# Optimization experiments

Measured on AMD Instinct MI355X. Metric: run time of the kernel, lower is better.

The kernel has to match this reference:

```python
import jax, jax.numpy as jnp
import numpy as np

B, T, D, H = 2, 2048, 1024, 16
DK = D // H

def setup_inputs() -> dict:
    key = jax.random.key(0)
    ks = jax.random.split(key, 12)
    s = 1.0 / np.sqrt(D)
    inp = {
        'Q': jax.random.normal(ks[0], (B, T, D), jnp.float32),
        'K': jax.random.normal(ks[1], (B, T, D), jnp.float32),
        'V': jax.random.normal(ks[2], (B, T, D), jnp.float32),
        'mask': jnp.tril(jnp.ones((T, T), jnp.int32))[None, None],  # causal [1,1,T,T]
        'Wq_w': jax.random.normal(ks[3], (D, D), jnp.float32) * s,
        'Wq_b': jax.random.normal(ks[4], (D,), jnp.float32) * s,
        'Wk_w': jax.random.normal(ks[5], (D, D), jnp.float32) * s,
        'Wk_b': jax.random.normal(ks[6], (D,), jnp.float32) * s,
        'Wv_w': jax.random.normal(ks[7], (D, D), jnp.float32) * s,
        'Wv_b': jax.random.normal(ks[8], (D,), jnp.float32) * s,
        'Wo_w': jax.random.normal(ks[9], (D, D), jnp.float32) * s,
        'Wo_b': jax.random.normal(ks[10], (D,), jnp.float32) * s,
    }
    return inp

def reference(Q, K, V, mask, Wq_w, Wq_b, Wk_w, Wk_b, Wv_w, Wv_b, Wo_w, Wo_b):
    b, tq, c = Q.shape
    tk = K.shape[1]
    q = (Q @ Wq_w + Wq_b).reshape(b, tq, H, DK).transpose(0, 2, 1, 3)  # [B,H,Tq,dk]
    k = (K @ Wk_w + Wk_b).reshape(b, tk, H, DK).transpose(0, 2, 1, 3)
    v = (V @ Wv_w + Wv_b).reshape(b, tk, H, DK).transpose(0, 2, 1, 3)
    scores = jnp.einsum('bhqd,bhkd->bhqk', q, k) / jnp.sqrt(jnp.float32(DK))
    scores = jnp.where(mask == 0, jnp.float32(-1e9), scores)
    attn = jax.nn.softmax(scores, axis=-1)
    out = jnp.einsum('bhqk,bhkd->bhqd', attn, v)
    out = out.transpose(0, 2, 1, 3).reshape(b, tq, c)
    return out @ Wo_w + Wo_b
```

## Files before the change

### kernel.cpp

```cpp
#include <hip/hip_runtime.h>
#include <hip/hip_bf16.h>

#define NB 2
#define NT 2048
#define ND 1024
#define NH 16
#define NDK 64

typedef __attribute__((ext_vector_type(8))) short bf16x8;
typedef __attribute__((ext_vector_type(4))) float f32x4;

#define VMCNT0 asm volatile("s_waitcnt vmcnt(0)" ::: "memory")
#define VMCNT3 asm volatile("s_waitcnt vmcnt(3)" ::: "memory")
#define VMCNT4 asm volatile("s_waitcnt vmcnt(4)" ::: "memory")

static __device__ __forceinline__ short f2bf(float f) {
  union { float f; unsigned u; } c; c.f = f;
  unsigned u = c.u;
  u += 0x7FFF + ((u >> 16) & 1);
  return (short)(u >> 16);
}

static __device__ __forceinline__ unsigned cvt_pk_bf16(float lo, float hi) {
  unsigned r;
  asm("v_cvt_pk_bf16_f32 %0, %1, %2" : "=v"(r) : "v"(lo), "v"(hi));
  return r;
}

static __device__ __forceinline__ void gload16(const void* g, void* l) {
  __builtin_amdgcn_global_load_lds((const __attribute__((address_space(1))) void*)g,
                                   (__attribute__((address_space(3))) void*)l, 16, 0, 0);
}

__global__ void prep_kernel(const float* __restrict__ Q, const float* __restrict__ Ki,
                            const float* __restrict__ V,
                            short* __restrict__ Qb, short* __restrict__ Kb, short* __restrict__ Vb,
                            const float* __restrict__ W0, const float* __restrict__ W1,
                            const float* __restrict__ W2, const float* __restrict__ W3,
                            short* __restrict__ T0, short* __restrict__ T1,
                            short* __restrict__ T2, short* __restrict__ T3) {
  __shared__ float t[32][33];
  int d = blockIdx.x, tid = threadIdx.x;
  if (d < 6144) {
    int z = d >> 11;
    int i = (d & 2047) * 256 + tid;
    const float* src = z == 0 ? Q : (z == 1 ? Ki : V);
    short* dst       = z == 0 ? Qb : (z == 1 ? Kb : Vb);
    const float4* s4 = (const float4*)src + (size_t)i * 2;
    float4 a = s4[0], b = s4[1];
    bf16x8 o;
    o[0] = f2bf(a.x); o[1] = f2bf(a.y); o[2] = f2bf(a.z); o[3] = f2bf(a.w);
    o[4] = f2bf(b.x); o[5] = f2bf(b.y); o[6] = f2bf(b.z); o[7] = f2bf(b.w);
    *((bf16x8*)dst + i) = o;
  } else {
    int dd = d - 6144;
    int z = dd >> 10;
    int rem = dd & 1023;
    const float* W = z == 0 ? W0 : (z == 1 ? W1 : (z == 2 ? W2 : W3));
    short* Wt      = z == 0 ? T0 : (z == 1 ? T1 : (z == 2 ? T2 : T3));
    int n0 = (rem & 31) * 32, k0 = (rem >> 5) * 32;
    int tx = tid & 31, ty = tid >> 5;
    for (int i = ty; i < 32; i += 8) t[i][tx] = W[(size_t)(k0 + i) * ND + n0 + tx];
    __syncthreads();
    for (int i = ty; i < 32; i += 8) Wt[(size_t)(n0 + i) * ND + k0 + tx] = f2bf(t[tx][i]);
  }
}

template <int MODE, int BN>
__global__ __launch_bounds__(256, 3) void gemm_bt(
    const short* __restrict__ A0, const short* __restrict__ A1, const short* __restrict__ A2,
    const short* __restrict__ W0, const short* __restrict__ W1, const short* __restrict__ W2,
    const float* __restrict__ b0, const float* __restrict__ b1, const float* __restrict__ b2,
    void* o0, void* o1, void* o2)
{
  constexpr int K = ND;
  constexpr int NK = K / 32;
  constexpr int NI = BN / 32;
  constexpr int NNB = ND / BN;
  constexpr int NZ = (MODE == 0) ? 3 : 1;
  constexpr int NWPX = NZ * 32 * NNB / 8;
  __shared__ short As[3][128 * 32];
  __shared__ short Bs[3][BN * 32];

  int d = blockIdx.x;
  int work = (d & 7) * NWPX + (d >> 3);
  int z = work / (32 * NNB);
  int rem = work % (32 * NNB);
  int m0 = (rem / NNB) * 128, n0 = (rem % NNB) * BN;

  const short* A    = z == 0 ? A0 : (z == 1 ? A1 : A2);
  const short* Wt   = z == 0 ? W0 : (z == 1 ? W1 : W2);
  const float* bias = z == 0 ? b0 : (z == 1 ? b1 : b2);
  void* out         = z == 0 ? o0 : (z == 1 ? o1 : o2);
  float scl = (MODE == 0 && z == 0) ? 0.18033688011112042f : 1.0f;

  int tid = threadIdx.x, wid = tid >> 6, lane = tid & 63;
  int wr = wid >> 1, wc = wid & 1;
  int r16 = lane & 15, l4 = lane >> 4;

  auto stage = [&](int buf, int kt) {
    int row = (lane >> 2);
    int c8 = (lane & 3) * 8;
    {
      int rbase = wid * 32;
      const short* ga = A + (size_t)(m0 + rbase + row) * K + kt * 32 + c8;
      gload16(ga,          &As[buf][rbase * 32]);
      gload16(ga + 16 * K, &As[buf][(rbase + 16) * 32]);
    }
    if constexpr (BN == 128) {
      int rbase = wid * 32;
      const short* gb = Wt + (size_t)(n0 + rbase + row) * K + kt * 32 + c8;
      gload16(gb,          &Bs[buf][rbase * 32]);
      gload16(gb + 16 * K, &Bs[buf][(rbase + 16) * 32]);
    } else {
      int rbase = wid * 16;
      const short* gb = Wt + (size_t)(n0 + rbase + row) * K + kt * 32 + c8;
      gload16(gb,          &Bs[buf][rbase * 32]);
    }
  };

  f32x4 acc[4][NI] = {};
  stage(0, 0);
  stage(1, 1);

  int cur = 0;
  for (int kt = 0; kt < NK; ++kt) {
    if (kt + 1 < NK) {
      if constexpr (BN == 128) VMCNT4; else VMCNT3;
    } else {
      VMCNT0;
    }
    __builtin_amdgcn_s_barrier();
    if (kt + 2 < NK) {
      int nb_ = cur + 2; if (nb_ >= 3) nb_ -= 3;
      stage(nb_, kt + 2);
    }
    bf16x8 af[4], bfv[NI];
    int kk = l4 * 8;
#pragma unroll
    for (int mi = 0; mi < 4; mi++)
      af[mi] = *(const bf16x8*)&As[cur][(wr * 64 + mi * 16 + r16) * 32 + kk];
#pragma unroll
    for (int ni = 0; ni < NI; ni++)
      bfv[ni] = *(const bf16x8*)&Bs[cur][(wc * (BN / 2) + ni * 16 + r16) * 32 + kk];
#pragma unroll
    for (int mi = 0; mi < 4; mi++)
#pragma unroll
      for (int ni = 0; ni < NI; ni++)
        acc[mi][ni] = __builtin_amdgcn_mfma_f32_16x16x32_bf16(af[mi], bfv[ni], acc[mi][ni], 0, 0, 0);
    cur = cur + 1; if (cur >= 3) cur = 0;
  }

  int mb = m0 + wr * 64, nb = n0 + wc * (BN / 2);

  if constexpr (MODE == 0) {
    if (z == 2) {
#pragma unroll
      for (int mi = 0; mi < 4; mi++)
#pragma unroll
        for (int ni = 0; ni < NI; ni++) {
          int n = nb + ni * 16 + r16;
          float bv = bias[n];
          int h = n >> 6, dk = n & 63;
          int m0_ = mb + mi * 16 + l4 * 4;
          int bI = m0_ >> 11, t0 = m0_ & (NT - 1);
          int bh = bI * NH + h;
          short4 s4;
          s4.x = f2bf(acc[mi][ni][0] + bv);
          s4.y = f2bf(acc[mi][ni][1] + bv);
          s4.z = f2bf(acc[mi][ni][2] + bv);
          s4.w = f2bf(acc[mi][ni][3] + bv);
          *(short4*)&((short*)out)[(size_t)bh * 131072 + (dk >> 4) * 32768 +
                                   (t0 >> 3) * 128 + (dk & 15) * 8 + (t0 & 7)] = s4;
        }
      return;
    }
  }

  __syncthreads();
  float* scr = (float*)&As[0][0] + wid * 320;
#pragma unroll
  for (int mi = 0; mi < 4; mi++)
#pragma unroll
    for (int ni = 0; ni < NI; ni++) {
#pragma unroll
      for (int r = 0; r < 4; r++)
        scr[(l4 * 4 + r) * 20 + r16] = acc[mi][ni][r];
      float4 tv = *(float4*)&scr[r16 * 20 + l4 * 4];
      int n0q = nb + ni * 16 + l4 * 4;
      float4 bv4 = *(const float4*)&bias[n0q];
      float v0 = tv.x + bv4.x, v1 = tv.y + bv4.y;
      float v2 = tv.z + bv4.z, v3 = tv.w + bv4.w;
      int m = mb + mi * 16 + r16;
      if constexpr (MODE == 0) {
        int bI = m >> 11, t = m & (NT - 1);
        if (z == 0) {
          int h = n0q >> 6, dk = n0q & 63;
          *(int2*)&((short*)out)[((((size_t)bI * NH + h) * NT + t) << 6) + dk] =
              make_int2((int)cvt_pk_bf16(v0 * scl, v1 * scl),
                        (int)cvt_pk_bf16(v2 * scl, v3 * scl));
        } else {
          int bh = bI * NH + (n0q >> 6);
          int dk = n0q & 63;
          *(int2*)&((short*)out)[(size_t)bh * 131072 + (t >> 4) * 1024 +
                                 (dk >> 3) * 128 + (t & 15) * 8 + (dk & 7)] =
              make_int2((int)cvt_pk_bf16(v0, v1), (int)cvt_pk_bf16(v2, v3));
        }
      } else {
        *(float4*)&((float*)out)[(size_t)m * ND + n0q] = make_float4(v0, v1, v2, v3);
      }
    }
}

__global__ __launch_bounds__(256) void attn_kernel(
    const short* __restrict__ q, const short* __restrict__ k, const short* __restrict__ vt,
    short* __restrict__ O)
{
  struct SH {
    union {
      short p2[4][2][16][72];
      struct {
        f32x4 obuf[4][2][2][64];
        float ol[4][32];
      } mg;
    };
  };
  __shared__ SH sh;

  int d = blockIdx.x;
  int xcd = d & 7, jj = d >> 3;
  int bh = xcd * 4 + (jj >> 6);
  int qg = 63 - (jj & 63);
  int b = bh >> 4, h = bh & 15;
  int tid = threadIdx.x, wid = tid >> 6, lane = tid & 63;
  int r16 = lane & 15, l4 = lane >> 4;
  size_t hb = (size_t)bh * NT * NDK;
  const short* qh = q + hb;
  const short* kh = k + hb;
  const short* vh = vt + hb;
  int qw = qg * 32;

  bf16x8 qa[2][2];
#pragma unroll
  for (int rf = 0; rf < 2; rf++)
#pragma unroll
    for (int kf = 0; kf < 2; kf++)
      qa[rf][kf] = *(const bf16x8*)(qh + (size_t)(qw + rf * 16 + r16) * NDK + kf * 32 + l4 * 8);

  f32x4 of[2][4] = {};
  float l0 = 0.f, l1 = 0.f;

  int nt = (qw + 95) >> 6;

  bf16x8 kfr[4][2];
  if (wid < nt) {
#pragma unroll
    for (int cf = 0; cf < 4; cf++) {
      const short* kb_ = kh + (size_t)((wid * 64 >> 4) + cf) * 1024 + lane * 8;
      kfr[cf][0] = *(const bf16x8*)kb_;
      kfr[cf][1] = *(const bf16x8*)(kb_ + 512);
    }
  }

  for (int kt = wid; kt < nt; kt += 4) {
    int kv0 = kt * 64;
    f32x4 sf[2][4] = {};

#pragma unroll
    for (int cf = 0; cf < 4; cf++) {
      sf[0][cf] = __builtin_amdgcn_mfma_f32_16x16x32_bf16(kfr[cf][0], qa[0][0], sf[0][cf], 0, 0, 0);
      sf[0][cf] = __builtin_amdgcn_mfma_f32_16x16x32_bf16(kfr[cf][1], qa[0][1], sf[0][cf], 0, 0, 0);
    }
#pragma unroll
    for (int cf = 0; cf < 4; cf++) {
      sf[1][cf] = __builtin_amdgcn_mfma_f32_16x16x32_bf16(kfr[cf][0], qa[1][0], sf[1][cf], 0, 0, 0);
      sf[1][cf] = __builtin_amdgcn_mfma_f32_16x16x32_bf16(kfr[cf][1], qa[1][1], sf[1][cf], 0, 0, 0);
    }

    {
      int ktn = (kt + 4 < nt) ? kt + 4 : kt;
      int kvn = ktn * 64;
#pragma unroll
      for (int cf = 0; cf < 4; cf++) {
        const short* kb_ = kh + (size_t)((kvn >> 4) + cf) * 1024 + lane * 8;
        kfr[cf][0] = *(const bf16x8*)kb_;
        kfr[cf][1] = *(const bf16x8*)(kb_ + 512);
      }
    }

    bf16x8 vb[4][2];
#pragma unroll
    for (int df = 0; df < 4; df++)
#pragma unroll
      for (int kf = 0; kf < 2; kf++)
        vb[df][kf] = *(const bf16x8*)(vh + df * 32768 + (kv0 >> 3) * 128 + kf * 512 + lane * 8);

    bool nm = (kv0 + 63 > qw);

    if (nm) {
#pragma unroll
      for (int cf = 0; cf < 4; cf++)
#pragma unroll
        for (int r = 0; r < 4; r++) {
          int kvi = kv0 + cf * 16 + l4 * 4 + r;
          if (kvi > qw + r16) sf[0][cf][r] = -1e30f;
        }
    }
    {
      float rs = 0.f;
#pragma unroll
      for (int cf = 0; cf < 4; cf++) {
        float p0 = __builtin_amdgcn_exp2f(sf[0][cf][0]);
        float p1 = __builtin_amdgcn_exp2f(sf[0][cf][1]);
        float p2v = __builtin_amdgcn_exp2f(sf[0][cf][2]);
        float p3 = __builtin_amdgcn_exp2f(sf[0][cf][3]);
        rs += (p0 + p1) + (p2v + p3);
        unsigned w0 = cvt_pk_bf16(p0, p1);
        unsigned w1 = cvt_pk_bf16(p2v, p3);
        *(int2*)&sh.p2[wid][0][r16][cf * 16 + l4 * 4] = make_int2((int)w0, (int)w1);
      }
      l0 += rs;
    }
#pragma unroll
    for (int kf = 0; kf < 2; kf++) {
      bf16x8 pa = *(const bf16x8*)&sh.p2[wid][0][r16][kf * 32 + l4 * 8];
#pragma unroll
      for (int df = 0; df < 4; df++)
        of[0][df] = __builtin_amdgcn_mfma_f32_16x16x32_bf16(vb[df][kf], pa, of[0][df], 0, 0, 0);
    }

    if (nm) {
#pragma unroll
      for (int cf = 0; cf < 4; cf++)
#pragma unroll
        for (int r = 0; r < 4; r++) {
          int kvi = kv0 + cf * 16 + l4 * 4 + r;
          if (kvi > qw + 16 + r16) sf[1][cf][r] = -1e30f;
        }
    }
    {
      float rs = 0.f;
#pragma unroll
      for (int cf = 0; cf < 4; cf++) {
        float p0 = __builtin_amdgcn_exp2f(sf[1][cf][0]);
        float p1 = __builtin_amdgcn_exp2f(sf[1][cf][1]);
        float p2v = __builtin_amdgcn_exp2f(sf[1][cf][2]);
        float p3 = __builtin_amdgcn_exp2f(sf[1][cf][3]);
        rs += (p0 + p1) + (p2v + p3);
        unsigned w0 = cvt_pk_bf16(p0, p1);
        unsigned w1 = cvt_pk_bf16(p2v, p3);
        *(int2*)&sh.p2[wid][1][r16][cf * 16 + l4 * 4] = make_int2((int)w0, (int)w1);
      }
      l1 += rs;
    }
#pragma unroll
    for (int kf = 0; kf < 2; kf++) {
      bf16x8 pa = *(const bf16x8*)&sh.p2[wid][1][r16][kf * 32 + l4 * 8];
#pragma unroll
      for (int df = 0; df < 4; df++)
        of[1][df] = __builtin_amdgcn_mfma_f32_16x16x32_bf16(vb[df][kf], pa, of[1][df], 0, 0, 0);
    }
  }

  l0 += __shfl_xor(l0, 16); l0 += __shfl_xor(l0, 32);
  l1 += __shfl_xor(l1, 16); l1 += __shfl_xor(l1, 32);

  __syncthreads();
  if (l4 == 0) {
    sh.mg.ol[wid][r16] = l0;
    sh.mg.ol[wid][16 + r16] = l1;
  }
#pragma unroll
  for (int pass = 0; pass < 2; ++pass) {
#pragma unroll
    for (int rf = 0; rf < 2; rf++)
#pragma unroll
      for (int dfp = 0; dfp < 2; dfp++)
        sh.mg.obuf[wid][rf][dfp][lane] = of[rf][2 * pass + dfp];
    __syncthreads();
    {
      int mrf = wid >> 1, mdfp = wid & 1, mdf = 2 * pass + mdfp;
      int row = mrf * 16 + r16;
      float lst = sh.mg.ol[0][row] + sh.mg.ol[1][row] + sh.mg.ol[2][row] + sh.mg.ol[3][row];
      float rinv = 1.0f / lst;
      f32x4 o0 = sh.mg.obuf[0][mrf][mdfp][lane];
      f32x4 o1 = sh.mg.obuf[1][mrf][mdfp][lane];
      f32x4 o2 = sh.mg.obuf[2][mrf][mdfp][lane];
      f32x4 o3 = sh.mg.obuf[3][mrf][mdfp][lane];
      float v0 = (o0[0] + o1[0] + o2[0] + o3[0]) * rinv;
      float v1 = (o0[1] + o1[1] + o2[1] + o3[1]) * rinv;
      float v2 = (o0[2] + o1[2] + o2[2] + o3[2]) * rinv;
      float v3 = (o0[3] + o1[3] + o2[3] + o3[3]) * rinv;
      int t = qw + mrf * 16 + r16;
      *(int2*)&O[(size_t)(b * NT + t) * ND + h * 64 + mdf * 16 + l4 * 4] =
          make_int2((int)cvt_pk_bf16(v0, v1), (int)cvt_pk_bf16(v2, v3));
    }
    __syncthreads();
  }
}

extern "C" void kernel_launch(void* const* d_in, const int* in_sizes, int n_in,
                              void* d_out, int out_size, void* d_ws, size_t ws_size,
                              hipStream_t stream)
{
  const float* Q  = (const float*)d_in[0];
  const float* Ki = (const float*)d_in[1];
  const float* V  = (const float*)d_in[2];
  const float* Wq = (const float*)d_in[4];  const float* bq = (const float*)d_in[5];
  const float* Wk = (const float*)d_in[6];  const float* bk = (const float*)d_in[7];
  const float* Wv = (const float*)d_in[8];  const float* bv = (const float*)d_in[9];
  const float* Wo = (const float*)d_in[10]; const float* bo = (const float*)d_in[11];

  short* ws = (short*)d_ws;
  const size_t M4 = (size_t)4 * 1024 * 1024;
  short* Qb  = ws;
  short* Kb  = ws + M4;
  short* Vb  = ws + 2 * M4;
  short* qp  = ws + 3 * M4;
  short* kp  = ws + 4 * M4;
  short* vtp = ws + 5 * M4;
  short* Wqt = ws + 6 * M4;
  short* Wkt = Wqt + 1024 * 1024;
  short* Wvt = Wkt + 1024 * 1024;
  short* Wot = Wvt + 1024 * 1024;
  short* Obuf = Qb;

  prep_kernel<<<10240, 256, 0, stream>>>(Q, Ki, V, Qb, Kb, Vb,
                                         Wq, Wk, Wv, Wo, Wqt, Wkt, Wvt, Wot);

  gemm_bt<0, 128><<<768, 256, 0, stream>>>(Qb, Kb, Vb, Wqt, Wkt, Wvt,
                                           bq, bk, bv, qp, kp, vtp);
  attn_kernel<<<2048, 256, 0, stream>>>(qp, kp, vtp, Obuf);
  gemm_bt<1, 64><<<512, 256, 0, stream>>>(Obuf, Obuf, Obuf, Wot, Wot, Wot,
                                          bo, bo, bo, d_out, d_out, d_out);
}
```

Before: 111.8 us.

## Process 64 query rows per attention block to reuse K/V tiles

Each attention workgroup now handles two 32-row query groups (64 rows) instead of one, so every K and V tile it loads feeds twice as many MFMAs, and the grid is halved to 1024 blocks. Causal masking is simplified to the single diagonal tile, and the final cross-wave merge loops over the two query groups. The aim is to halve K/V global traffic per query. The cost is more registers (doubled Q fragments and accumulators), which may lower occupancy, and fewer blocks, which gives coarser load balance.

```diff
diff --git a/kernel.cpp b/kernel.cpp
--- a/kernel.cpp
+++ b/kernel.cpp
@@ -229,8 +229,8 @@
 
   int d = blockIdx.x;
   int xcd = d & 7, jj = d >> 3;
-  int bh = xcd * 4 + (jj >> 6);
-  int qg = 63 - (jj & 63);
+  int bh = xcd * 4 + (jj >> 5);
+  int g = 31 - (jj & 31);
   int b = bh >> 4, h = bh & 15;
   int tid = threadIdx.x, wid = tid >> 6, lane = tid & 63;
   int r16 = lane & 15, l4 = lane >> 4;
@@ -238,25 +238,27 @@
   const short* qh = q + hb;
   const short* kh = k + hb;
   const short* vh = vt + hb;
-  int qw = qg * 32;
-
-  bf16x8 qa[2][2];
-#pragma unroll
-  for (int rf = 0; rf < 2; rf++)
-#pragma unroll
-    for (int kf = 0; kf < 2; kf++)
-      qa[rf][kf] = *(const bf16x8*)(qh + (size_t)(qw + rf * 16 + r16) * NDK + kf * 32 + l4 * 8);
-
-  f32x4 of[2][4] = {};
-  float l0 = 0.f, l1 = 0.f;
-
-  int nt = (qw + 95) >> 6;
+  int qwb = g * 64;
+  int nt = g + 1;
+
+  bf16x8 qa[2][2][2];
+#pragma unroll
+  for (int qgi = 0; qgi < 2; qgi++)
+#pragma unroll
+    for (int rf = 0; rf < 2; rf++)
+#pragma unroll
+      for (int kf = 0; kf < 2; kf++)
+        qa[qgi][rf][kf] = *(const bf16x8*)(qh + (size_t)(qwb + qgi * 32 + rf * 16 + r16) * NDK +
+                                           kf * 32 + l4 * 8);
+
+  f32x4 of[2][2][4] = {};
+  float l00 = 0.f, l01 = 0.f, l10 = 0.f, l11 = 0.f;
 
   bf16x8 kfr[4][2];
   if (wid < nt) {
 #pragma unroll
     for (int cf = 0; cf < 4; cf++) {
-      const short* kb_ = kh + (size_t)((wid * 64 >> 4) + cf) * 1024 + lane * 8;
+      const short* kb_ = kh + (size_t)(wid * 4 + cf) * 1024 + lane * 8;
       kfr[cf][0] = *(const bf16x8*)kb_;
       kfr[cf][1] = *(const bf16x8*)(kb_ + 512);
     }
@@ -264,138 +266,152 @@
 
   for (int kt = wid; kt < nt; kt += 4) {
     int kv0 = kt * 64;
-    f32x4 sf[2][4] = {};
-
-#pragma unroll
-    for (int cf = 0; cf < 4; cf++) {
-      sf[0][cf] = __builtin_amdgcn_mfma_f32_16x16x32_bf16(kfr[cf][0], qa[0][0], sf[0][cf], 0, 0, 0);
-      sf[0][cf] = __builtin_amdgcn_mfma_f32_16x16x32_bf16(kfr[cf][1], qa[0][1], sf[0][cf], 0, 0, 0);
-    }
-#pragma unroll
-    for (int cf = 0; cf < 4; cf++) {
-      sf[1][cf] = __builtin_amdgcn_mfma_f32_16x16x32_bf16(kfr[cf][0], qa[1][0], sf[1][cf], 0, 0, 0);
-      sf[1][cf] = __builtin_amdgcn_mfma_f32_16x16x32_bf16(kfr[cf][1], qa[1][1], sf[1][cf], 0, 0, 0);
-    }
+    bool nm = (kt == g);
+
+    bf16x8 vb[4][2];
+#pragma unroll
+    for (int df = 0; df < 4; df++)
+#pragma unroll
+      for (int kf = 0; kf < 2; kf++)
+        vb[df][kf] = *(const bf16x8*)(vh + df * 32768 + (kv0 >> 3) * 128 + kf * 512 + lane * 8);
+
+    f32x4 sf[2][4];
+
+#pragma unroll
+    for (int rf = 0; rf < 2; rf++)
+#pragma unroll
+      for (int cf = 0; cf < 4; cf++) {
+        f32x4 zz = {};
+        zz = __builtin_amdgcn_mfma_f32_16x16x32_bf16(kfr[cf][0], qa[0][rf][0], zz, 0, 0, 0);
+        sf[rf][cf] = __builtin_amdgcn_mfma_f32_16x16x32_bf16(kfr[cf][1], qa[0][rf][1], zz, 0, 0, 0);
+      }
+    if (nm) {
+#pragma unroll
+      for (int rf = 0; rf < 2; rf++)
+#pragma unroll
+        for (int cf = 0; cf < 4; cf++)
+#pragma unroll
+          for (int r = 0; r < 4; r++) {
+            int kvi = kv0 + cf * 16 + l4 * 4 + r;
+            if (kvi > qwb + rf * 16 + r16) sf[rf][cf][r] = -1e30f;
+          }
+    }
+#pragma unroll
+    for (int rf = 0; rf < 2; rf++) {
+      float rs = 0.f;
+#pragma unroll
+      for (int cf = 0; cf < 4; cf++) {
+        float p0 = __builtin_amdgcn_exp2f(sf[rf][cf][0]);
+        float p1 = __builtin_amdgcn_exp2f(sf[rf][cf][1]);
+        float p2v = __builtin_amdgcn_exp2f(sf[rf][cf][2]);
+        float p3 = __builtin_amdgcn_exp2f(sf[rf][cf][3]);
+        rs += (p0 + p1) + (p2v + p3);
+        *(int2*)&sh.p2[wid][rf][r16][cf * 16 + l4 * 4] =
+            make_int2((int)cvt_pk_bf16(p0, p1), (int)cvt_pk_bf16(p2v, p3));
+      }
+      if (rf == 0) l00 += rs; else l01 += rs;
+#pragma unroll
+      for (int kf = 0; kf < 2; kf++) {
+        bf16x8 pa = *(const bf16x8*)&sh.p2[wid][rf][r16][kf * 32 + l4 * 8];
+#pragma unroll
+        for (int df = 0; df < 4; df++)
+          of[0][rf][df] = __builtin_amdgcn_mfma_f32_16x16x32_bf16(vb[df][kf], pa, of[0][rf][df], 0, 0, 0);
+      }
+    }
+
+#pragma unroll
+    for (int rf = 0; rf < 2; rf++)
+#pragma unroll
+      for (int cf = 0; cf < 4; cf++) {
+        f32x4 zz = {};
+        zz = __builtin_amdgcn_mfma_f32_16x16x32_bf16(kfr[cf][0], qa[1][rf][0], zz, 0, 0, 0);
+        sf[rf][cf] = __builtin_amdgcn_mfma_f32_16x16x32_bf16(kfr[cf][1], qa[1][rf][1], zz, 0, 0, 0);
+      }
 
     {
       int ktn = (kt + 4 < nt) ? kt + 4 : kt;
-      int kvn = ktn * 64;
 #pragma unroll
       for (int cf = 0; cf < 4; cf++) {
-        const short* kb_ = kh + (size_t)((kvn >> 4) + cf) * 1024 + lane * 8;
+        const short* kb_ = kh + (size_t)(ktn * 4 + cf) * 1024 + lane * 8;
         kfr[cf][0] = *(const bf16x8*)kb_;
         kfr[cf][1] = *(const bf16x8*)(kb_ + 512);
       }
     }
 
-    bf16x8 vb[4][2];
-#pragma unroll
-    for (int df = 0; df < 4; df++)
-#pragma unroll
-      for (int kf = 0; kf < 2; kf++)
-        vb[df][kf] = *(const bf16x8*)(vh + df * 32768 + (kv0 >> 3) * 128 + kf * 512 + lane * 8);
-
-    bool nm = (kv0 + 63 > qw);
-
     if (nm) {
 #pragma unroll
-      for (int cf = 0; cf < 4; cf++)
-#pragma unroll
-        for (int r = 0; r < 4; r++) {
-          int kvi = kv0 + cf * 16 + l4 * 4 + r;
-          if (kvi > qw + r16) sf[0][cf][r] = -1e30f;
-        }
-    }
-    {
+      for (int rf = 0; rf < 2; rf++)
+#pragma unroll
+        for (int cf = 0; cf < 4; cf++)
+#pragma unroll
+          for (int r = 0; r < 4; r++) {
+            int kvi = kv0 + cf * 16 + l4 * 4 + r;
+            if (kvi > qwb + 32 + rf * 16 + r16) sf[rf][cf][r] = -1e30f;
+          }
+    }
+#pragma unroll
+    for (int rf = 0; rf < 2; rf++) {
       float rs = 0.f;
 #pragma unroll
       for (int cf = 0; cf < 4; cf++) {
-        float p0 = __builtin_amdgcn_exp2f(sf[0][cf][0]);
-        float p1 = __builtin_amdgcn_exp2f(sf[0][cf][1]);
-        float p2v = __builtin_amdgcn_exp2f(sf[0][cf][2]);
-        float p3 = __builtin_amdgcn_exp2f(sf[0][cf][3]);
+        float p0 = __builtin_amdgcn_exp2f(sf[rf][cf][0]);
+        float p1 = __builtin_amdgcn_exp2f(sf[rf][cf][1]);
+        float p2v = __builtin_amdgcn_exp2f(sf[rf][cf][2]);
+        float p3 = __builtin_amdgcn_exp2f(sf[rf][cf][3]);
         rs += (p0 + p1) + (p2v + p3);
-        unsigned w0 = cvt_pk_bf16(p0, p1);
-        unsigned w1 = cvt_pk_bf16(p2v, p3);
-        *(int2*)&sh.p2[wid][0][r16][cf * 16 + l4 * 4] = make_int2((int)w0, (int)w1);
-      }
-      l0 += rs;
-    }
-#pragma unroll
-    for (int kf = 0; kf < 2; kf++) {
-      bf16x8 pa = *(const bf16x8*)&sh.p2[wid][0][r16][kf * 32 + l4 * 8];
-#pragma unroll
-      for (int df = 0; df < 4; df++)
-        of[0][df] = __builtin_amdgcn_mfma_f32_16x16x32_bf16(vb[df][kf], pa, of[0][df], 0, 0, 0);
-    }
-
-    if (nm) {
-#pragma unroll
-      for (int cf = 0; cf < 4; cf++)
-#pragma unroll
-        for (int r = 0; r < 4; r++) {
-          int kvi = kv0 + cf * 16 + l4 * 4 + r;
-          if (kvi > qw + 16 + r16) sf[1][cf][r] = -1e30f;
-        }
-    }
-    {
-      float rs = 0.f;
-#pragma unroll
-      for (int cf = 0; cf < 4; cf++) {
-        float p0 = __builtin_amdgcn_exp2f(sf[1][cf][0]);
-        float p1 = __builtin_amdgcn_exp2f(sf[1][cf][1]);
-        float p2v = __builtin_amdgcn_exp2f(sf[1][cf][2]);
-        float p3 = __builtin_amdgcn_exp2f(sf[1][cf][3]);
-        rs += (p0 + p1) + (p2v + p3);
-        unsigned w0 = cvt_pk_bf16(p0, p1);
-        unsigned w1 = cvt_pk_bf16(p2v, p3);
-        *(int2*)&sh.p2[wid][1][r16][cf * 16 + l4 * 4] = make_int2((int)w0, (int)w1);
-      }
-      l1 += rs;
-    }
-#pragma unroll
-    for (int kf = 0; kf < 2; kf++) {
-      bf16x8 pa = *(const bf16x8*)&sh.p2[wid][1][r16][kf * 32 + l4 * 8];
-#pragma unroll
-      for (int df = 0; df < 4; df++)
-        of[1][df] = __builtin_amdgcn_mfma_f32_16x16x32_bf16(vb[df][kf], pa, of[1][df], 0, 0, 0);
-    }
-  }
-
-  l0 += __shfl_xor(l0, 16); l0 += __shfl_xor(l0, 32);
-  l1 += __shfl_xor(l1, 16); l1 += __shfl_xor(l1, 32);
-
-  __syncthreads();
-  if (l4 == 0) {
-    sh.mg.ol[wid][r16] = l0;
-    sh.mg.ol[wid][16 + r16] = l1;
-  }
-#pragma unroll
-  for (int pass = 0; pass < 2; ++pass) {
-#pragma unroll
-    for (int rf = 0; rf < 2; rf++)
-#pragma unroll
-      for (int dfp = 0; dfp < 2; dfp++)
-        sh.mg.obuf[wid][rf][dfp][lane] = of[rf][2 * pass + dfp];
+        *(int2*)&sh.p2[wid][rf][r16][cf * 16 + l4 * 4] =
+            make_int2((int)cvt_pk_bf16(p0, p1), (int)cvt_pk_bf16(p2v, p3));
+      }
+      if (rf == 0) l10 += rs; else l11 += rs;
+#pragma unroll
+      for (int kf = 0; kf < 2; kf++) {
+        bf16x8 pa = *(const bf16x8*)&sh.p2[wid][rf][r16][kf * 32 + l4 * 8];
+#pragma unroll
+        for (int df = 0; df < 4; df++)
+          of[1][rf][df] = __builtin_amdgcn_mfma_f32_16x16x32_bf16(vb[df][kf], pa, of[1][rf][df], 0, 0, 0);
+      }
+    }
+  }
+
+  l00 += __shfl_xor(l00, 16); l00 += __shfl_xor(l00, 32);
+  l01 += __shfl_xor(l01, 16); l01 += __shfl_xor(l01, 32);
+  l10 += __shfl_xor(l10, 16); l10 += __shfl_xor(l10, 32);
+  l11 += __shfl_xor(l11, 16); l11 += __shfl_xor(l11, 32);
+
+#pragma unroll 1
+  for (int qgi = 0; qgi < 2; ++qgi) {
     __syncthreads();
-    {
-      int mrf = wid >> 1, mdfp = wid & 1, mdf = 2 * pass + mdfp;
-      int row = mrf * 16 + r16;
-      float lst = sh.mg.ol[0][row] + sh.mg.ol[1][row] + sh.mg.ol[2][row] + sh.mg.ol[3][row];
-      float rinv = 1.0f / lst;
-      f32x4 o0 = sh.mg.obuf[0][mrf][mdfp][lane];
-      f32x4 o1 = sh.mg.obuf[1][mrf][mdfp][lane];
-      f32x4 o2 = sh.mg.obuf[2][mrf][mdfp][lane];
-      f32x4 o3 = sh.mg.obuf[3][mrf][mdfp][lane];
-      float v0 = (o0[0] + o1[0] + o2[0] + o3[0]) * rinv;
-      float v1 = (o0[1] + o1[1] + o2[1] + o3[1]) * rinv;
-      float v2 = (o0[2] + o1[2] + o2[2] + o3[2]) * rinv;
-      float v3 = (o0[3] + o1[3] + o2[3] + o3[3]) * rinv;
-      int t = qw + mrf * 16 + r16;
-      *(int2*)&O[(size_t)(b * NT + t) * ND + h * 64 + mdf * 16 + l4 * 4] =
-          make_int2((int)cvt_pk_bf16(v0, v1), (int)cvt_pk_bf16(v2, v3));
-    }
-    __syncthreads();
+    if (l4 == 0) {
+      sh.mg.ol[wid][r16]      = qgi == 0 ? l00 : l10;
+      sh.mg.ol[wid][16 + r16] = qgi == 0 ? l01 : l11;
+    }
+#pragma unroll
+    for (int pass = 0; pass < 2; ++pass) {
+#pragma unroll
+      for (int rf = 0; rf < 2; rf++)
+#pragma unroll
+        for (int dfp = 0; dfp < 2; dfp++)
+          sh.mg.obuf[wid][rf][dfp][lane] = of[qgi][rf][2 * pass + dfp];
+      __syncthreads();
+      {
+        int mrf = wid >> 1, mdfp = wid & 1, mdf = 2 * pass + mdfp;
+        int row = mrf * 16 + r16;
+        float lst = sh.mg.ol[0][row] + sh.mg.ol[1][row] + sh.mg.ol[2][row] + sh.mg.ol[3][row];
+        float rinv = 1.0f / lst;
+        f32x4 o0 = sh.mg.obuf[0][mrf][mdfp][lane];
+        f32x4 o1 = sh.mg.obuf[1][mrf][mdfp][lane];
+        f32x4 o2 = sh.mg.obuf[2][mrf][mdfp][lane];
+        f32x4 o3 = sh.mg.obuf[3][mrf][mdfp][lane];
+        float v0 = (o0[0] + o1[0] + o2[0] + o3[0]) * rinv;
+        float v1 = (o0[1] + o1[1] + o2[1] + o3[1]) * rinv;
+        float v2 = (o0[2] + o1[2] + o2[2] + o3[2]) * rinv;
+        float v3 = (o0[3] + o1[3] + o2[3] + o3[3]) * rinv;
+        int t = qwb + qgi * 32 + mrf * 16 + r16;
+        *(int2*)&O[(size_t)(b * NT + t) * ND + h * 64 + mdf * 16 + l4 * 4] =
+            make_int2((int)cvt_pk_bf16(v0, v1), (int)cvt_pk_bf16(v2, v3));
+      }
+      __syncthreads();
+    }
   }
 }
 
@@ -430,7 +446,7 @@
 
   gemm_bt<0, 128><<<768, 256, 0, stream>>>(Qb, Kb, Vb, Wqt, Wkt, Wvt,
                                            bq, bk, bv, qp, kp, vtp);
-  attn_kernel<<<2048, 256, 0, stream>>>(qp, kp, vtp, Obuf);
+  attn_kernel<<<1024, 256, 0, stream>>>(qp, kp, vtp, Obuf);
   gemm_bt<1, 64><<<512, 256, 0, stream>>>(Obuf, Obuf, Obuf, Wot, Wot, Wot,
                                           bo, bo, bo, d_out, d_out, d_out);
 }
```

New measurement: 137.2 us. 1.23x slower.
